# Kernel tuning notes

Measured on AMD Instinct MI355X. Metric: run time of the kernel, lower is better.

Reference implementation:

```python
import jax, jax.numpy as jnp
import numpy as np

B, S, H = 8, 8192, 1024
CAPACITY_FACTOR = 0.5


def setup_inputs() -> dict:
    key = jax.random.key(0)
    ks = jax.random.split(key, 5)
    sc = lambda fan: np.float32(1.0 / np.sqrt(fan))
    return {
        "x": jax.random.normal(ks[0], (B, S, H), dtype=jnp.float32),
        # router: Linear(H, H//4) -> ReLU -> Linear(H//4, 1)
        "W1": jax.random.normal(ks[1], (H, H // 4), dtype=jnp.float32) * sc(H),
        "b1": jnp.zeros((H // 4,), dtype=jnp.float32),
        "W2": jax.random.normal(ks[2], (H // 4, 1), dtype=jnp.float32) * sc(H // 4),
        "b2": jnp.zeros((1,), dtype=jnp.float32),
        # external layer_fn realized as a dense layer: gelu(x @ Wl)
        "Wl": jax.random.normal(ks[3], (H, H), dtype=jnp.float32) * sc(H),
    }


def reference(x, W1, b1, W2, b2, Wl):
    # router scores [B, S, 1]
    scores = jax.nn.relu(jnp.einsum("bsh,hd->bsd", x, W1) + b1)
    scores = jnp.einsum("bsd,do->bso", scores, W2) + b2
    routing_weights = jax.nn.sigmoid(scores)  # [B, S, 1]

    # eval path: process only top-capacity tokens per batch row
    capacity = int(S * CAPACITY_FACTOR)
    _, top_idx = jax.lax.top_k(scores[..., 0], capacity)  # [B, C]

    selected = jnp.take_along_axis(x, top_idx[..., None], axis=1)  # [B, C, H]
    processed = jax.nn.gelu(jnp.einsum("bch,hd->bcd", selected, Wl))  # layer_fn

    batch_idx = jnp.arange(x.shape[0])[:, None]  # [B, 1]
    output = x.at[batch_idx, top_idx].set(processed)  # scatter back into clone of x
    return output, routing_weights
```

## Files before the change

kernel.cpp:

```cpp
#include <hip/hip_runtime.h>
#include <stdint.h>

#define B_   8
#define S_   8192
#define H_   1024
#define HQ_  256
#define CAP_ 4096
#define UCAP_ (S_-CAP_)
#define M_   (B_*CAP_)
#define EPSB 0.012f
#define LCAP 8192

using f32x4 = __attribute__((ext_vector_type(4))) float;
using s16x8 = __attribute__((ext_vector_type(8))) short;

__device__ __forceinline__ unsigned short f2bf(float f) {
  unsigned u = __float_as_uint(f);
  u += 0x7FFF + ((u >> 16) & 1);
  return (unsigned short)(u >> 16);
}
__device__ __forceinline__ float bf2f(unsigned short h) {
  return __uint_as_float(((unsigned)h) << 16);
}

__device__ __forceinline__ float gelu_f(float v) {
  float s = v + 0.044715f * v * v * v;
  float e = __expf(-1.5957691216057308f * s);
  return v * __builtin_amdgcn_rcpf(1.0f + e);
}

__device__ __forceinline__ unsigned mono(float f) {
  unsigned u = __float_as_uint(f);
  return (u & 0x80000000u) ? ~u : (u | 0x80000000u);
}
__device__ __forceinline__ float unmono(unsigned k) {
  unsigned u = (k & 0x80000000u) ? (k & 0x7fffffffu) : ~k;
  return __uint_as_float(u);
}

__device__ __forceinline__ void gload_lds16(const void* g, void* l) {
  __builtin_amdgcn_global_load_lds(
      (const __attribute__((address_space(1))) void*)(uintptr_t)g,
      (__attribute__((address_space(3))) void*)(uintptr_t)l,
      16, 0, 0);
}

__global__ __launch_bounds__(256) void prep_w1_kernel(
    const float* __restrict__ W1, unsigned short* __restrict__ w1t_hi) {
  __shared__ float tile[32][33];
  const int n0 = blockIdx.x * 32, k0 = blockIdx.y * 32;
  const int tx = threadIdx.x, ty = threadIdx.y;
  for (int i = ty; i < 32; i += 8) tile[i][tx] = W1[(size_t)(k0 + i) * HQ_ + n0 + tx];
  __syncthreads();
  for (int i = ty; i < 32; i += 8)
    w1t_hi[(size_t)(n0 + i) * H_ + k0 + tx] = f2bf(tile[tx][i]);
}

__global__ __launch_bounds__(512) void router_mfma_kernel(
    const float* __restrict__ x, const unsigned short* __restrict__ w1t_hi,
    const float* __restrict__ b1, const float* __restrict__ W2,
    const float* __restrict__ b2, float* __restrict__ scores,
    float* __restrict__ rw) {
  __shared__ __align__(16) unsigned short AsH[128 * 64];
  __shared__ __align__(16) unsigned short BsH[256 * 64];
  __shared__ float part[128][4];
  const int t = threadIdx.x;
  const int lane = t & 63, w = t >> 6;
  const int m0 = blockIdx.x * 128;
  const int wr = w >> 2, wc = w & 3;
  const int r16 = lane & 15, ks = lane >> 4;

  const float* aptr[4];
  int aso[4];
  #pragma unroll
  for (int u = 0; u < 4; ++u) {
    int idx = t + u * 512;
    int row = idx >> 4, q = idx & 15;
    aptr[u] = x + (size_t)(m0 + row) * H_ + q * 4;
    aso[u] = row * 64 + (((q >> 1) ^ (row & 7)) << 3) + (q & 1) * 4;
  }
  const unsigned short* bptr[4];
  int bdst[4];
  #pragma unroll
  for (int u = 0; u < 4; ++u) {
    int c0 = u * 512 + w * 64;
    int c = c0 + lane;
    int row = c >> 3, sl = c & 7;
    int slz = sl ^ (row & 7);
    bptr[u] = w1t_hi + (size_t)row * H_ + slz * 8;
    bdst[u] = c0 * 8;
  }

  f32x4 acc[4][4];
  #pragma unroll
  for (int i = 0; i < 4; ++i)
    #pragma unroll
    for (int j = 0; j < 4; ++j) acc[i][j] = (f32x4){0.f, 0.f, 0.f, 0.f};

  for (int k0 = 0; k0 < H_; k0 += 64) {
    float4 av[4];
    #pragma unroll
    for (int u = 0; u < 4; ++u) av[u] = *(const float4*)(aptr[u] + k0);
    #pragma unroll
    for (int u = 0; u < 4; ++u) gload_lds16(bptr[u] + k0, &BsH[bdst[u]]);
    #pragma unroll
    for (int u = 0; u < 4; ++u) {
      ushort4 hh;
      hh.x = f2bf(av[u].x); hh.y = f2bf(av[u].y);
      hh.z = f2bf(av[u].z); hh.w = f2bf(av[u].w);
      *(ushort4*)&AsH[aso[u]] = hh;
    }
    __syncthreads();
    #pragma unroll
    for (int kk = 0; kk < 2; ++kk) {
      const int g = kk * 4 + ks;
      s16x8 ah[4], bh[4];
      #pragma unroll
      for (int i = 0; i < 4; ++i) {
        int r = wr * 64 + i * 16 + r16;
        ah[i] = *(const s16x8*)&AsH[r * 64 + (g ^ (r & 7)) * 8];
      }
      #pragma unroll
      for (int j = 0; j < 4; ++j) {
        int r = wc * 64 + j * 16 + r16;
        bh[j] = *(const s16x8*)&BsH[r * 64 + (g ^ (r & 7)) * 8];
      }
      #pragma unroll
      for (int i = 0; i < 4; ++i)
        #pragma unroll
        for (int j = 0; j < 4; ++j)
          acc[i][j] = __builtin_amdgcn_mfma_f32_16x16x32_bf16(ah[i], bh[j], acc[i][j], 0, 0, 0);
    }
    __syncthreads();
  }

  float b1v[4], w2v[4];
  #pragma unroll
  for (int j = 0; j < 4; ++j) {
    int n = wc * 64 + j * 16 + r16;
    b1v[j] = b1[n]; w2v[j] = W2[n];
  }
  const int g4 = lane >> 4;
  #pragma unroll
  for (int i = 0; i < 4; ++i) {
    #pragma unroll
    for (int r = 0; r < 4; ++r) {
      float p = 0.f;
      #pragma unroll
      for (int j = 0; j < 4; ++j) {
        float h = acc[i][j][r] + b1v[j];
        h = fmaxf(h, 0.f);
        p = fmaf(h, w2v[j], p);
      }
      p += __shfl_xor(p, 1);
      p += __shfl_xor(p, 2);
      p += __shfl_xor(p, 4);
      p += __shfl_xor(p, 8);
      if (r16 == 0) part[wr * 64 + i * 16 + g4 * 4 + r][wc] = p;
    }
  }
  __syncthreads();
  if (t < 128) {
    float sc = part[t][0] + part[t][1] + part[t][2] + part[t][3] + b2[0];
    scores[m0 + t] = sc;
    rw[m0 + t] = 1.f / (1.f + expf(-sc));
  }
}

__global__ __launch_bounds__(1024) void select_kernel(
    const float* __restrict__ scores, float* __restrict__ thr) {
  __shared__ unsigned hist[2048];
  __shared__ unsigned sh_b, sh_gt;
  const int b = blockIdx.x;
  const int tid = threadIdx.x;
  const float* srow = scores + (size_t)b * S_;
  unsigned prefix = 0; int plen = 0; unsigned rank = CAP_;
  #pragma unroll
  for (int round = 0; round < 3; ++round) {
    const int nb = (round < 2) ? 11 : 10;
    hist[tid] = 0; hist[tid + 1024] = 0;
    __syncthreads();
    for (int i = tid; i < S_; i += 1024) {
      unsigned k = mono(srow[i]);
      if (plen == 0 || (k >> (32 - plen)) == prefix) {
        unsigned bucket = (k << plen) >> (32 - nb);
        atomicAdd(&hist[bucket], 1u);
      }
    }
    __syncthreads();
    for (int s = 1; s < 2048; s <<= 1) {
      unsigned t0 = (tid + s < 2048) ? hist[tid + s] : 0;
      unsigned t1 = (tid + 1024 + s < 2048) ? hist[tid + 1024 + s] : 0;
      __syncthreads();
      hist[tid] += t0; hist[tid + 1024] += t1;
      __syncthreads();
    }
    #pragma unroll
    for (int h = 0; h < 2; ++h) {
      int i = tid + h * 1024;
      unsigned ge = hist[i];
      unsigned gt = (i < 2047) ? hist[i + 1] : 0;
      if (gt < rank && rank <= ge) { sh_b = (unsigned)i; sh_gt = gt; }
    }
    __syncthreads();
    prefix = (prefix << nb) | sh_b;
    plen += nb;
    rank -= sh_gt;
    __syncthreads();
  }
  if (tid == 0) thr[b] = unmono(prefix);
}

__global__ __launch_bounds__(256) void band_kernel(
    const float* __restrict__ scores, const float* __restrict__ thr,
    int* __restrict__ list, int* __restrict__ count) {
  int i = blockIdx.x * 256 + threadIdx.x;
  float s = scores[i];
  int b = i >> 13;
  if (fabsf(s - thr[b]) <= EPSB) {
    int p = atomicAdd(count, 1);
    if (p < LCAP) list[p] = i;
  }
}

__global__ __launch_bounds__(256) void recompute_kernel(
    const float* __restrict__ x, const float* __restrict__ W1,
    const float* __restrict__ b1, const float* __restrict__ W2,
    const float* __restrict__ b2, const int* __restrict__ list,
    const int* __restrict__ count, float* __restrict__ scores,
    float* __restrict__ rw) {
  __shared__ float xr[4][H_];
  __shared__ float red[4][4];
  int n = *count; if (n > LCAP) n = LCAP;
  const int j = threadIdx.x;
  for (int base = blockIdx.x * 4; base < n; base += gridDim.x * 4) {
    int nt = n - base; if (nt > 4) nt = 4;
    for (int tt = 0; tt < 4; ++tt) {
      int tok = list[base + ((tt < nt) ? tt : 0)];
      const float* xrow = x + (size_t)tok * H_;
      for (int k = j; k < H_; k += 256) xr[tt][k] = xrow[k];
    }
    __syncthreads();
    float a0 = 0.f, a1 = 0.f, a2 = 0.f, a3 = 0.f;
    for (int k = 0; k < H_; ++k) {
      float wv = W1[(size_t)k * HQ_ + j];
      a0 = fmaf(xr[0][k], wv, a0);
      a1 = fmaf(xr[1][k], wv, a1);
      a2 = fmaf(xr[2][k], wv, a2);
      a3 = fmaf(xr[3][k], wv, a3);
    }
    float aa[4] = {a0, a1, a2, a3};
    #pragma unroll
    for (int tt = 0; tt < 4; ++tt) {
      float h = fmaxf(aa[tt] + b1[j], 0.f);
      float v = h * W2[j];
      v += __shfl_xor(v, 1);  v += __shfl_xor(v, 2);  v += __shfl_xor(v, 4);
      v += __shfl_xor(v, 8);  v += __shfl_xor(v, 16); v += __shfl_xor(v, 32);
      if ((j & 63) == 0) red[tt][j >> 6] = v;
    }
    __syncthreads();
    if (j < nt) {
      int tok = list[base + j];
      float sc = red[j][0] + red[j][1] + red[j][2] + red[j][3] + b2[0];
      scores[tok] = sc;
      rw[tok] = 1.f / (1.f + expf(-sc));
    }
    __syncthreads();
  }
}

__global__ __launch_bounds__(1024) void compact_kernel(
    const float* __restrict__ scores, const float* __restrict__ thr,
    int* __restrict__ comp, int* __restrict__ ucomp) {
  __shared__ int wc_eq[16], wc_sel[16], red[16];
  const int b = blockIdx.x;
  const float T = thr[b];
  const float* srow = scores + (size_t)b * S_;
  const int tid = threadIdx.x, lane = tid & 63, wid = tid >> 6;

  int cgt = 0;
  #pragma unroll
  for (int c = 0; c < 8; ++c) cgt += (srow[c * 1024 + tid] > T) ? 1 : 0;
  cgt += __shfl_xor(cgt, 1);  cgt += __shfl_xor(cgt, 2);  cgt += __shfl_xor(cgt, 4);
  cgt += __shfl_xor(cgt, 8);  cgt += __shfl_xor(cgt, 16); cgt += __shfl_xor(cgt, 32);
  if (lane == 0) red[wid] = cgt;
  __syncthreads();
  int cnt_gt = 0;
  #pragma unroll
  for (int i = 0; i < 16; ++i) cnt_gt += red[i];
  const int need = CAP_ - cnt_gt;

  int* crow = comp + b * CAP_;
  int* urow = ucomp + b * UCAP_;
  int sel_base = 0, unsel_base = 0, eq_base = 0;
  __syncthreads();
  for (int c = 0; c < 8; ++c) {
    int idx = c * 1024 + tid;
    float s = srow[idx];
    bool gt = s > T, eq = (s == T);
    unsigned long long meq = __ballot(eq);
    if (lane == 0) wc_eq[wid] = __popcll(meq);
    __syncthreads();
    int eq_off = eq_base, eq_tot = 0;
    #pragma unroll
    for (int w2 = 0; w2 < 16; ++w2) { if (w2 < wid) eq_off += wc_eq[w2]; eq_tot += wc_eq[w2]; }
    int eqpos = eq_off + __popcll(meq & ((1ull << lane) - 1));
    bool take = gt || (eq && eqpos < need);
    unsigned long long mt = __ballot(take);
    if (lane == 0) wc_sel[wid] = __popcll(mt);
    __syncthreads();
    int sel_off = sel_base, sel_tot = 0;
    #pragma unroll
    for (int w2 = 0; w2 < 16; ++w2) { if (w2 < wid) sel_off += wc_sel[w2]; sel_tot += wc_sel[w2]; }
    if (take) {
      crow[sel_off + __popcll(mt & ((1ull << lane) - 1))] = idx;
    } else {
      int un_off = unsel_base + wid * 64 - (sel_off - sel_base);
      urow[un_off + __popcll(~mt & ((1ull << lane) - 1))] = idx;
    }
    sel_base += sel_tot; unsel_base += 1024 - sel_tot; eq_base += eq_tot;
    __syncthreads();
  }
}

__global__ __launch_bounds__(256) void copy_unsel_kernel(
    const float* __restrict__ x, const int* __restrict__ ucomp,
    float* __restrict__ out) {
  int i = blockIdx.x;
  int b = i >> 12, r = i & (UCAP_ - 1);
  int token = ucomp[b * UCAP_ + r];
  size_t row = (size_t)b * S_ + token;
  const float4* src = (const float4*)(x + row * H_);
  float4* dst = (float4*)(out + row * H_);
  dst[threadIdx.x] = src[threadIdx.x];
}

__global__ __launch_bounds__(256) void wlt_kernel(
    const float* __restrict__ wl, unsigned short* __restrict__ wlt) {
  __shared__ float tile[32][33];
  const int x0 = blockIdx.x * 32, y0 = blockIdx.y * 32;
  const int tx = threadIdx.x, ty = threadIdx.y;
  for (int i = ty; i < 32; i += 8) tile[i][tx] = wl[(size_t)(y0 + i) * H_ + x0 + tx];
  __syncthreads();
  for (int i = ty; i < 32; i += 8)
    wlt[(size_t)(x0 + i) * H_ + y0 + tx] = f2bf(tile[tx][i]);
}

__global__ __launch_bounds__(256) void gather_cast_kernel(
    const float* __restrict__ x, const int* __restrict__ comp,
    unsigned short* __restrict__ xg) {
  int tid = blockIdx.x * 256 + threadIdx.x;
  int rowc = tid >> 8;
  int c4 = tid & 255;
  int b = rowc >> 12, cc = rowc & (CAP_ - 1);
  int token = comp[b * CAP_ + cc];
  float4 v = *(const float4*)&x[((size_t)(b * S_ + token)) * H_ + c4 * 4];
  ushort4 o;
  o.x = f2bf(v.x); o.y = f2bf(v.y); o.z = f2bf(v.z); o.w = f2bf(v.w);
  *(ushort4*)&xg[(size_t)rowc * H_ + c4 * 4] = o;
}

#define ISSUE_A(P, KT, BUF) do {                                               \
    int row_ = half * 128 + (P) * 32 + rr;                                     \
    int slz_ = sl ^ (row_ & 7);                                                \
    gload_lds16(xg + (size_t)(m0 + row_) * H_ + (KT) * 64 + slz_ * 8,          \
                &As[BUF][row_ * 64 + sl * 8]);                                 \
  } while (0)
#define ISSUE_B(P, KT, BUF) do {                                               \
    int row_ = half * 128 + (P) * 32 + rr;                                     \
    int slz_ = sl ^ (row_ & 7);                                                \
    gload_lds16(wlt + (size_t)(n0 + row_) * H_ + (KT) * 64 + slz_ * 8,         \
                &Bs[BUF][row_ * 64 + sl * 8]);                                 \
  } while (0)
#define MOE_PHASE(P, ISSUE, WAITSTR) do {                                      \
    s16x8 af[2][2];                                                            \
    _Pragma("unroll")                                                          \
    for (int i = 0; i < 2; ++i)                                                \
      _Pragma("unroll")                                                        \
      for (int kk = 0; kk < 2; ++kk) {                                         \
        int r_ = wr * 128 + (2 * (P) + i) * 16 + r16;                          \
        af[i][kk] = *(const s16x8*)&As[c_][r_ * 64 + ((kk * 4 + ks) ^ (r_ & 7)) * 8]; \
      }                                                                        \
    if ((P) == 0) {                                                            \
      _Pragma("unroll")                                                        \
      for (int j = 0; j < 4; ++j)                                              \
        _Pragma("unroll")                                                      \
        for (int kk = 0; kk < 2; ++kk) {                                       \
          int r_ = wc * 64 + j * 16 + r16;                                     \
          bfr[j][kk] = *(const s16x8*)&Bs[c_][r_ * 64 + ((kk * 4 + ks) ^ (r_ & 7)) * 8]; \
        }                                                                      \
    }                                                                          \
    ISSUE                                                                      \
    __builtin_amdgcn_s_barrier();                                              \
    asm volatile("s_waitcnt lgkmcnt(0)" ::: "memory");                         \
    __builtin_amdgcn_sched_barrier(0);                                         \
    __builtin_amdgcn_s_setprio(1);                                             \
    _Pragma("unroll")                                                          \
    for (int i = 0; i < 2; ++i)                                                \
      _Pragma("unroll")                                                        \
      for (int j = 0; j < 4; ++j)                                              \
        _Pragma("unroll")                                                      \
        for (int kk = 0; kk < 2; ++kk)                                         \
          acc[2 * (P) + i][j] = __builtin_amdgcn_mfma_f32_16x16x32_bf16(       \
              af[i][kk], bfr[j][kk], acc[2 * (P) + i][j], 0, 0, 0);            \
    __builtin_amdgcn_s_setprio(0);                                             \
    __builtin_amdgcn_sched_barrier(0);                                         \
    asm volatile("s_waitcnt " WAITSTR ::: "memory");                           \
    __builtin_amdgcn_s_barrier();                                              \
    __builtin_amdgcn_sched_barrier(0);                                         \
  } while (0)

__global__ __launch_bounds__(512, 1) void moe_gemm_kernel(
    const unsigned short* __restrict__ xg, const unsigned short* __restrict__ wlt,
    const int* __restrict__ comp, float* __restrict__ out) {
  __shared__ __align__(16) unsigned short As[2][256 * 64];
  __shared__ __align__(16) unsigned short Bs[2][256 * 64];
  __shared__ int toks[256];
  const int t = threadIdx.x;
  const int lane = t & 63, w = t >> 6;
  const int bid = blockIdx.x;
  const int xcd = bid & 7, wb = bid >> 3;
  const int m0 = (xcd * 16 + (wb >> 2)) * 256;
  const int n0 = (wb & 3) * 256;
  const int bb = m0 >> 12;
  if (t < 256) toks[t] = comp[bb * CAP_ + (m0 & (CAP_ - 1)) + t];
  const int wr = w >> 2, wc = w & 3;
  const int r16 = lane & 15, ks = lane >> 4;
  const int half = t >> 8, rr = (t >> 3) & 31, sl = t & 7;

  f32x4 acc[8][4];
  #pragma unroll
  for (int i = 0; i < 8; ++i)
    #pragma unroll
    for (int j = 0; j < 4; ++j) acc[i][j] = (f32x4){0.f, 0.f, 0.f, 0.f};

  ISSUE_B(0, 0, 0); ISSUE_B(1, 0, 0); ISSUE_B(2, 0, 0); ISSUE_B(3, 0, 0);
  ISSUE_A(0, 0, 0); ISSUE_A(1, 0, 0); ISSUE_A(2, 0, 0); ISSUE_A(3, 0, 0);
  asm volatile("s_waitcnt vmcnt(3)" ::: "memory");
  __syncthreads();

  for (int kt = 0; kt < 15; ++kt) {
    const int c_ = kt & 1, nb_ = c_ ^ 1;
    const int kn = kt + 1;
    s16x8 bfr[4][2];
    MOE_PHASE(0, { ISSUE_B(0, kn, nb_); ISSUE_B(1, kn, nb_); }, "vmcnt(4)");
    MOE_PHASE(1, { ISSUE_B(2, kn, nb_); ISSUE_B(3, kn, nb_); }, "vmcnt(5)");
    MOE_PHASE(2, { ISSUE_A(0, kn, nb_); ISSUE_A(1, kn, nb_); }, "vmcnt(6)");
    MOE_PHASE(3, { ISSUE_A(2, kn, nb_); ISSUE_A(3, kn, nb_); }, "vmcnt(3)");
  }
  {
    const int c_ = 1;
    s16x8 bfr[4][2];
    MOE_PHASE(0, {;}, "vmcnt(2)");
    MOE_PHASE(1, {;}, "vmcnt(1)");
    MOE_PHASE(2, {;}, "vmcnt(0)");
    MOE_PHASE(3, {;}, "vmcnt(63)");
  }

  const int g4 = lane >> 4;
  #pragma unroll
  for (int i = 0; i < 8; ++i) {
    #pragma unroll
    for (int r = 0; r < 4; ++r) {
      int rl = wr * 128 + i * 16 + g4 * 4 + r;
      int token = toks[rl];
      float* orow = out + ((size_t)(bb * S_ + token)) * H_ + n0 + wc * 64;
      #pragma unroll
      for (int j = 0; j < 4; ++j)
        orow[j * 16 + r16] = gelu_f(acc[i][j][r]);
    }
  }
}

extern "C" void kernel_launch(void* const* d_in, const int* in_sizes, int n_in,
                              void* d_out, int out_size, void* d_ws, size_t ws_size,
                              hipStream_t stream) {
  const float* x  = (const float*)d_in[0];
  const float* W1 = (const float*)d_in[1];
  const float* b1 = (const float*)d_in[2];
  const float* W2 = (const float*)d_in[3];
  const float* b2 = (const float*)d_in[4];
  const float* Wl = (const float*)d_in[5];
  float* out = (float*)d_out;
  float* rw  = out + (size_t)B_ * S_ * H_;

  char* ws = (char*)d_ws;
  float* scores        = (float*)ws;
  int*   comp          = (int*)(ws + (256 << 10));
  float* thr           = (float*)(ws + (384 << 10));
  int*   count         = (int*)(ws + (384 << 10) + 256);
  int*   list          = (int*)(ws + (384 << 10) + 512);
  int*   ucomp         = (int*)(ws + (448 << 10));
  unsigned short* wlt  = (unsigned short*)(ws + (1 << 20));
  unsigned short* xg   = (unsigned short*)(ws + (3 << 20));
  unsigned short* w1t_hi = xg;

  hipMemsetAsync(count, 0, sizeof(int), stream);
  hipLaunchKernelGGL(prep_w1_kernel, dim3(HQ_/32, H_/32), dim3(32, 8), 0, stream,
                     W1, w1t_hi);
  hipLaunchKernelGGL(router_mfma_kernel, dim3((B_*S_)/128), dim3(512), 0, stream,
                     x, w1t_hi, b1, W2, b2, scores, rw);
  hipLaunchKernelGGL(select_kernel, dim3(B_), dim3(1024), 0, stream, scores, thr);
  hipLaunchKernelGGL(band_kernel, dim3((B_*S_)/256), dim3(256), 0, stream,
                     scores, thr, list, count);
  hipLaunchKernelGGL(recompute_kernel, dim3(128), dim3(256), 0, stream,
                     x, W1, b1, W2, b2, list, count, scores, rw);
  hipLaunchKernelGGL(select_kernel, dim3(B_), dim3(1024), 0, stream, scores, thr);
  hipLaunchKernelGGL(compact_kernel, dim3(B_), dim3(1024), 0, stream,
                     scores, thr, comp, ucomp);
  hipLaunchKernelGGL(copy_unsel_kernel, dim3(B_*UCAP_), dim3(256), 0, stream,
                     x, ucomp, out);
  hipLaunchKernelGGL(wlt_kernel, dim3(H_/32, H_/32), dim3(32, 8), 0, stream, Wl, wlt);
  hipLaunchKernelGGL(gather_cast_kernel, dim3(M_*H_/4/256), dim3(256), 0, stream,
                     x, comp, xg);
  hipLaunchKernelGGL(moe_gemm_kernel, dim3((M_/256)*(H_/256)), dim3(512), 0, stream,
                     xg, wlt, comp, out);
}
```

Measured before the change: 398.4 us.

## Double-buffer router GEMM with 256-row tiles and phased prefetch

Rewrites the router MFMA kernel to process 256 rows per block instead of 128, reusing each W1 tile across twice as many rows. LDS is double-buffered and the main loop is split into four phases, so the global loads for the next K tile are issued and written to LDS while MFMAs run on the current tile. It adds explicit barriers, waitcnts, sched_barrier and setprio hints. In exchange, accumulator registers double and LDS use grows to about 128KB, which limits the kernel to one block per CU, and the grid halves to 256 blocks.

```diff
diff --git a/kernel.cpp b/kernel.cpp
--- a/kernel.cpp
+++ b/kernel.cpp
@@ -56,82 +56,111 @@
     w1t_hi[(size_t)(n0 + i) * H_ + k0 + tx] = f2bf(tile[tx][i]);
 }
 
-__global__ __launch_bounds__(512) void router_mfma_kernel(
+#define RISSUE_B(P, KT, BUF) do {                                              \
+    int row_ = (P) * 64 + rr64;                                                \
+    int slz_ = slc ^ (row_ & 7);                                               \
+    gload_lds16(w1t_hi + (size_t)row_ * H_ + (KT) * 64 + slz_ * 8,             \
+                &BsR[BUF][row_ * 64 + slc * 8]);                               \
+  } while (0)
+#define RLOAD_A(V, KT) do {                                                    \
+    int idx_ = (V) * 512 + t;                                                  \
+    int row_ = idx_ >> 4, q_ = idx_ & 15;                                      \
+    av[V] = *(const float4*)&x[(size_t)(m0 + row_) * H_ + (KT) * 64 + q_ * 4]; \
+  } while (0)
+#define RWRITE_A(V, BUF) do {                                                  \
+    int idx_ = (V) * 512 + t;                                                  \
+    int row_ = idx_ >> 4, q_ = idx_ & 15;                                      \
+    int so_ = row_ * 64 + (((q_ >> 1) ^ (row_ & 7)) << 3) + (q_ & 1) * 4;      \
+    ushort4 hh;                                                                \
+    hh.x = f2bf(av[V].x); hh.y = f2bf(av[V].y);                                \
+    hh.z = f2bf(av[V].z); hh.w = f2bf(av[V].w);                                \
+    *(ushort4*)&AsR[BUF][so_] = hh;                                            \
+  } while (0)
+#define RPHASE(P, ISSUE, TAIL) do {                                            \
+    s16x8 af[2][2];                                                            \
+    _Pragma("unroll")                                                          \
+    for (int i = 0; i < 2; ++i)                                                \
+      _Pragma("unroll")                                                        \
+      for (int kk = 0; kk < 2; ++kk) {                                         \
+        int r_ = wr * 128 + (2 * (P) + i) * 16 + r16;                          \
+        af[i][kk] = *(const s16x8*)&AsR[c_][r_ * 64 + ((kk * 4 + ks) ^ (r_ & 7)) * 8]; \
+      }                                                                        \
+    if ((P) == 0) {                                                            \
+      _Pragma("unroll")                                                        \
+      for (int j = 0; j < 4; ++j)                                              \
+        _Pragma("unroll")                                                      \
+        for (int kk = 0; kk < 2; ++kk) {                                       \
+          int r_ = wc * 64 + j * 16 + r16;                                     \
+          bfr[j][kk] = *(const s16x8*)&BsR[c_][r_ * 64 + ((kk * 4 + ks) ^ (r_ & 7)) * 8]; \
+        }                                                                      \
+    }                                                                          \
+    ISSUE                                                                      \
+    __builtin_amdgcn_s_barrier();                                              \
+    asm volatile("s_waitcnt lgkmcnt(0)" ::: "memory");                         \
+    __builtin_amdgcn_sched_barrier(0);                                         \
+    __builtin_amdgcn_s_setprio(1);                                             \
+    _Pragma("unroll")                                                          \
+    for (int i = 0; i < 2; ++i)                                                \
+      _Pragma("unroll")                                                        \
+      for (int j = 0; j < 4; ++j)                                              \
+        _Pragma("unroll")                                                      \
+        for (int kk = 0; kk < 2; ++kk)                                         \
+          acc[2 * (P) + i][j] = __builtin_amdgcn_mfma_f32_16x16x32_bf16(       \
+              af[i][kk], bfr[j][kk], acc[2 * (P) + i][j], 0, 0, 0);            \
+    __builtin_amdgcn_s_setprio(0);                                             \
+    __builtin_amdgcn_sched_barrier(0);                                         \
+    TAIL                                                                       \
+    __builtin_amdgcn_s_barrier();                                              \
+    __builtin_amdgcn_sched_barrier(0);                                         \
+  } while (0)
+
+__global__ __launch_bounds__(512, 1) void router_mfma_kernel(
     const float* __restrict__ x, const unsigned short* __restrict__ w1t_hi,
     const float* __restrict__ b1, const float* __restrict__ W2,
     const float* __restrict__ b2, float* __restrict__ scores,
     float* __restrict__ rw) {
-  __shared__ __align__(16) unsigned short AsH[128 * 64];
-  __shared__ __align__(16) unsigned short BsH[256 * 64];
-  __shared__ float part[128][4];
+  __shared__ __align__(16) unsigned short AsR[2][256 * 64];
+  __shared__ __align__(16) unsigned short BsR[2][256 * 64];
+  __shared__ float part[256][4];
   const int t = threadIdx.x;
   const int lane = t & 63, w = t >> 6;
-  const int m0 = blockIdx.x * 128;
+  const int m0 = blockIdx.x * 256;
   const int wr = w >> 2, wc = w & 3;
   const int r16 = lane & 15, ks = lane >> 4;
-
-  const float* aptr[4];
-  int aso[4];
-  #pragma unroll
-  for (int u = 0; u < 4; ++u) {
-    int idx = t + u * 512;
-    int row = idx >> 4, q = idx & 15;
-    aptr[u] = x + (size_t)(m0 + row) * H_ + q * 4;
-    aso[u] = row * 64 + (((q >> 1) ^ (row & 7)) << 3) + (q & 1) * 4;
-  }
-  const unsigned short* bptr[4];
-  int bdst[4];
-  #pragma unroll
-  for (int u = 0; u < 4; ++u) {
-    int c0 = u * 512 + w * 64;
-    int c = c0 + lane;
-    int row = c >> 3, sl = c & 7;
-    int slz = sl ^ (row & 7);
-    bptr[u] = w1t_hi + (size_t)row * H_ + slz * 8;
-    bdst[u] = c0 * 8;
-  }
-
-  f32x4 acc[4][4];
-  #pragma unroll
-  for (int i = 0; i < 4; ++i)
+  const int rr64 = (t >> 3) & 63, slc = t & 7;
+
+  f32x4 acc[8][4];
+  #pragma unroll
+  for (int i = 0; i < 8; ++i)
     #pragma unroll
     for (int j = 0; j < 4; ++j) acc[i][j] = (f32x4){0.f, 0.f, 0.f, 0.f};
 
-  for (int k0 = 0; k0 < H_; k0 += 64) {
-    float4 av[4];
-    #pragma unroll
-    for (int u = 0; u < 4; ++u) av[u] = *(const float4*)(aptr[u] + k0);
-    #pragma unroll
-    for (int u = 0; u < 4; ++u) gload_lds16(bptr[u] + k0, &BsH[bdst[u]]);
-    #pragma unroll
-    for (int u = 0; u < 4; ++u) {
-      ushort4 hh;
-      hh.x = f2bf(av[u].x); hh.y = f2bf(av[u].y);
-      hh.z = f2bf(av[u].z); hh.w = f2bf(av[u].w);
-      *(ushort4*)&AsH[aso[u]] = hh;
-    }
-    __syncthreads();
-    #pragma unroll
-    for (int kk = 0; kk < 2; ++kk) {
-      const int g = kk * 4 + ks;
-      s16x8 ah[4], bh[4];
-      #pragma unroll
-      for (int i = 0; i < 4; ++i) {
-        int r = wr * 64 + i * 16 + r16;
-        ah[i] = *(const s16x8*)&AsH[r * 64 + (g ^ (r & 7)) * 8];
-      }
-      #pragma unroll
-      for (int j = 0; j < 4; ++j) {
-        int r = wc * 64 + j * 16 + r16;
-        bh[j] = *(const s16x8*)&BsH[r * 64 + (g ^ (r & 7)) * 8];
-      }
-      #pragma unroll
-      for (int i = 0; i < 4; ++i)
-        #pragma unroll
-        for (int j = 0; j < 4; ++j)
-          acc[i][j] = __builtin_amdgcn_mfma_f32_16x16x32_bf16(ah[i], bh[j], acc[i][j], 0, 0, 0);
-    }
-    __syncthreads();
+  float4 av[8];
+  RISSUE_B(0, 0, 0); RISSUE_B(1, 0, 0); RISSUE_B(2, 0, 0); RISSUE_B(3, 0, 0);
+  #pragma unroll
+  for (int v = 0; v < 8; ++v) RLOAD_A(v, 0);
+  #pragma unroll
+  for (int v = 0; v < 8; ++v) RWRITE_A(v, 0);
+  __syncthreads();
+
+  for (int kt = 0; kt < 16; ++kt) {
+    const int c_ = kt & 1, nb_ = c_ ^ 1;
+    const int kn = kt + 1;
+    const bool pf = (kt < 15);
+    s16x8 bfr[4][2];
+    RPHASE(0,
+      { if (pf) { RISSUE_B(0, kn, nb_); RISSUE_B(1, kn, nb_);
+                  _Pragma("unroll") for (int v = 0; v < 8; ++v) RLOAD_A(v, kn); } },
+      {;});
+    RPHASE(1,
+      { if (pf) { RISSUE_B(2, kn, nb_); RISSUE_B(3, kn, nb_); } },
+      {;});
+    RPHASE(2, {;},
+      { if (pf) { _Pragma("unroll") for (int v = 0; v < 4; ++v) RWRITE_A(v, nb_);
+                  asm volatile("s_waitcnt lgkmcnt(0)" ::: "memory"); } });
+    RPHASE(3, {;},
+      { if (pf) { _Pragma("unroll") for (int v = 4; v < 8; ++v) RWRITE_A(v, nb_);
+                  asm volatile("s_waitcnt vmcnt(0) lgkmcnt(0)" ::: "memory"); } });
   }
 
   float b1v[4], w2v[4];
@@ -142,7 +171,7 @@
   }
   const int g4 = lane >> 4;
   #pragma unroll
-  for (int i = 0; i < 4; ++i) {
+  for (int i = 0; i < 8; ++i) {
     #pragma unroll
     for (int r = 0; r < 4; ++r) {
       float p = 0.f;
@@ -156,11 +185,11 @@
       p += __shfl_xor(p, 2);
       p += __shfl_xor(p, 4);
       p += __shfl_xor(p, 8);
-      if (r16 == 0) part[wr * 64 + i * 16 + g4 * 4 + r][wc] = p;
-    }
-  }
-  __syncthreads();
-  if (t < 128) {
+      if (r16 == 0) part[wr * 128 + i * 16 + g4 * 4 + r][wc] = p;
+    }
+  }
+  __syncthreads();
+  if (t < 256) {
     float sc = part[t][0] + part[t][1] + part[t][2] + part[t][3] + b2[0];
     scores[m0 + t] = sc;
     rw[m0 + t] = 1.f / (1.f + expf(-sc));
@@ -498,7 +527,7 @@
   hipMemsetAsync(count, 0, sizeof(int), stream);
   hipLaunchKernelGGL(prep_w1_kernel, dim3(HQ_/32, H_/32), dim3(32, 8), 0, stream,
                      W1, w1t_hi);
-  hipLaunchKernelGGL(router_mfma_kernel, dim3((B_*S_)/128), dim3(512), 0, stream,
+  hipLaunchKernelGGL(router_mfma_kernel, dim3((B_*S_)/256), dim3(512), 0, stream,
                      x, w1t_hi, b1, W2, b2, scores, rw);
   hipLaunchKernelGGL(select_kernel, dim3(B_), dim3(1024), 0, stream, scores, thr);
   hipLaunchKernelGGL(band_kernel, dim3((B_*S_)/256), dim3(256), 0, stream,
```

Measured after the change: 443.6 us. 11.4% more time.
